# Kernel tuning notes

Measured on AMD Instinct MI355X. Metric: run time of the kernel, lower is better.

Reference implementation:

```python
import jax, jax.numpy as jnp
import numpy as np

NEG_SLOPE = 0.2


def setup_inputs() -> dict:
    key = jax.random.key(0)
    ks = jax.random.split(key, 9)
    N, E, D, H, C, G = 50000, 800000, 128, 4, 32, 64
    x = jax.random.normal(ks[0], (N, D), dtype=jnp.float32)
    edge_index = jax.random.randint(ks[1], (2, E), 0, N, dtype=jnp.int64)
    batch_ids = jnp.sort(jax.random.randint(ks[2], (N,), 0, G, dtype=jnp.int64))
    Wl = jax.random.normal(ks[3], (D, H * C), dtype=jnp.float32) / np.sqrt(D)
    Wr = jax.random.normal(ks[4], (D, H * C), dtype=jnp.float32) / np.sqrt(D)
    att = jax.random.normal(ks[5], (H, C), dtype=jnp.float32) / np.sqrt(C)
    bias_conv = jax.random.normal(ks[6], (H * C,), dtype=jnp.float32) * 0.01
    W_mlp = jax.random.normal(ks[7], (H * C, H * C), dtype=jnp.float32) / np.sqrt(H * C)
    b_mlp = jax.random.normal(ks[8], (H * C,), dtype=jnp.float32) * 0.01
    return {"x": x, "edge_index": edge_index, "batch_ids": batch_ids,
            "num_graphs": G, "Wl": Wl, "Wr": Wr, "att": att,
            "bias_conv": bias_conv, "W_mlp": W_mlp, "b_mlp": b_mlp}


def gatv2_forward(x, edge_index, batch_ids, num_graphs, Wl, Wr, att, bias_conv, W_mlp, b_mlp):
    N = x.shape[0]
    H, C = att.shape
    # add self loops (PyG default)
    loops = jnp.arange(N, dtype=edge_index.dtype)
    src = jnp.concatenate([edge_index[0], loops])
    dst = jnp.concatenate([edge_index[1], loops])
    xl = (x @ Wl).reshape(N, H, C)  # source transform
    xr = (x @ Wr).reshape(N, H, C)  # target transform
    # GATv2 attention logits per edge/head
    e = jax.nn.leaky_relu(xl[src] + xr[dst], NEG_SLOPE)  # [E,H,C]
    logits = jnp.einsum('ehc,hc->eh', e, att)            # [E,H]
    # segment softmax over incoming edges of each dst node
    m = jax.ops.segment_max(logits, dst, num_segments=N)
    ex = jnp.exp(logits - m[dst])
    denom = jax.ops.segment_sum(ex, dst, num_segments=N)
    alpha = ex / denom[dst]                              # [E,H]
    # weighted scatter-sum of source features
    out = jax.ops.segment_sum(alpha[:, :, None] * xl[src], dst, num_segments=N)
    out = out.reshape(N, H * C) + bias_conv
    out = jax.nn.relu(out)
    # global max pool per graph
    pooled = jax.ops.segment_max(out, batch_ids, num_segments=num_graphs)
    return jax.nn.relu(pooled @ W_mlp + b_mlp)


def reference(x, edge_index, batch_ids, num_graphs, Wl, Wr, att, bias_conv, W_mlp, b_mlp):
    return gatv2_forward(x, edge_index, batch_ids, num_graphs, Wl, Wr, att,
                         bias_conv, W_mlp, b_mlp)
```

## Files before the change

kernel.cpp:

```cpp
#include <hip/hip_runtime.h>
#include <hip/hip_bf16.h>

#define NN 50000
#define EE 800000
#define HC 128
#define GG 64

#define NBLK 256
#define CHUNK (EE / NBLK)
#define NBUCK ((NN + 63) >> 6)
#define NTOT (NBUCK * NBLK)
#define NSB ((NTOT + 1023) / 1024)
#define ECAP 2048

typedef __attribute__((ext_vector_type(8))) short bf16x8;
typedef __attribute__((ext_vector_type(4))) float f32x4;
typedef _Float16 hv2 __attribute__((ext_vector_type(2)));

__device__ __forceinline__ float dpp4_redrow(float t) {
  t += __int_as_float(__builtin_amdgcn_update_dpp(0, __float_as_int(t), 0x111, 0xf, 0xf, true));
  t += __int_as_float(__builtin_amdgcn_update_dpp(0, __float_as_int(t), 0x112, 0xf, 0xf, true));
  t += __int_as_float(__builtin_amdgcn_update_dpp(0, __float_as_int(t), 0x114, 0xf, 0xf, true));
  t += __int_as_float(__builtin_amdgcn_update_dpp(0, __float_as_int(t), 0x118, 0xf, 0xf, true));
  return t;
}
__device__ __forceinline__ float bcast15(float t) {
  return __int_as_float(__builtin_amdgcn_ds_swizzle(__float_as_int(t), 0x1F0));
}

__device__ __forceinline__ unsigned pkbf(float lo, float hi) {
  __hip_bfloat162 h = __float22bfloat162_rn(float2{lo, hi});
  return *reinterpret_cast<unsigned*>(&h);
}

__global__ __launch_bounds__(128) void prep_w(const float* __restrict__ Wl,
                                              const float* __restrict__ Wr,
                                              short* __restrict__ Wtb) {
  int c = blockIdx.x;
  int k = threadIdx.x;
  const float* W = (c < 128) ? Wl : Wr;
  float v = W[k * 128 + (c & 127)];
  Wtb[c * 128 + k] = (short)(pkbf(v, 0.f) & 0xFFFF);
}

__global__ __launch_bounds__(256) void gemm_xw(
    const float* __restrict__ x, const short* __restrict__ Wtb,
    _Float16* __restrict__ xlh, _Float16* __restrict__ xrh,
    const int* __restrict__ ei, int* __restrict__ H2T)
{
  __shared__ short xs[128 * 136];
  __shared__ int h[NBUCK];
  const int t = threadIdx.x;
  const int rowbase = blockIdx.x * 128;
#pragma unroll
  for (int i = 0; i < 16; ++i) {
    int fi = i * 256 + t;
    int row = fi >> 5, k4 = fi & 31;
    int ar = rowbase + row; if (ar >= NN) ar = NN - 1;
    float4 v = *(const float4*)(x + (size_t)ar * 128 + k4 * 4);
    uint2 p = { pkbf(v.x, v.y), pkbf(v.z, v.w) };
    *(uint2*)&xs[row * 136 + k4 * 4] = p;
  }
  __syncthreads();
  const int w = t >> 6, l = t & 63;
  const int lo16 = l & 15, hi = l >> 4;
  f32x4 accL[2][8], accR[2][8];
#pragma unroll
  for (int rf = 0; rf < 2; ++rf)
#pragma unroll
    for (int cf = 0; cf < 8; ++cf) {
      accL[rf][cf] = f32x4{0.f, 0.f, 0.f, 0.f};
      accR[rf][cf] = f32x4{0.f, 0.f, 0.f, 0.f};
    }

  const short* asrc0 = &xs[(w * 32 + lo16) * 136 + hi * 8];
  const short* asrc1 = asrc0 + 16 * 136;
#pragma unroll
  for (int ks = 0; ks < 4; ++ks) {
    bf16x8 a0 = *(const bf16x8*)(asrc0 + ks * 32);
    bf16x8 a1 = *(const bf16x8*)(asrc1 + ks * 32);
#pragma unroll
    for (int cf = 0; cf < 8; ++cf) {
      const short* bp = &Wtb[(cf * 16 + lo16) * 128 + ks * 32 + hi * 8];
      bf16x8 bL = *(const bf16x8*)bp;
      bf16x8 bR = *(const bf16x8*)(bp + 128 * 128);
      accL[0][cf] = __builtin_amdgcn_mfma_f32_16x16x32_bf16(a0, bL, accL[0][cf], 0, 0, 0);
      accL[1][cf] = __builtin_amdgcn_mfma_f32_16x16x32_bf16(a1, bL, accL[1][cf], 0, 0, 0);
      accR[0][cf] = __builtin_amdgcn_mfma_f32_16x16x32_bf16(a0, bR, accR[0][cf], 0, 0, 0);
      accR[1][cf] = __builtin_amdgcn_mfma_f32_16x16x32_bf16(a1, bR, accR[1][cf], 0, 0, 0);
    }
  }
#pragma unroll
  for (int rf = 0; rf < 2; ++rf)
#pragma unroll
    for (int cf = 0; cf < 8; ++cf)
#pragma unroll
      for (int r = 0; r < 4; ++r) {
        int row = rowbase + w * 32 + rf * 16 + hi * 4 + r;
        if (row < NN) {
          int col = cf * 16 + lo16;
          xlh[(size_t)row * 128 + col] = (_Float16)accL[rf][cf][r];
          xrh[(size_t)row * 128 + col] = (_Float16)accR[rf][cf][r];
        }
      }
  int blk = blockIdx.x;
  if (blk < NBLK) {
    for (int b = t; b < NBUCK; b += 256) h[b] = 0;
    __syncthreads();
    int e0 = blk * CHUNK;
    for (int i = t; i < CHUNK; i += 256) {
      int d = ei[EE + e0 + i];
      atomicAdd(&h[d >> 6], 1);
    }
    __syncthreads();
    for (int b = t; b < NBUCK; b += 256) H2T[b * NBLK + blk] = h[b];
  }
}

__global__ __launch_bounds__(256) void scanA(const int* __restrict__ H2T,
                                             int* __restrict__ PS, int* __restrict__ bsum) {
  __shared__ int tmp[256];
  int t = threadIdx.x;
  int base = blockIdx.x * 1024 + t * 4;
  int4 v = {0, 0, 0, 0};
  if (base < NTOT) v = *(const int4*)&H2T[base];
  int local = v.x + v.y + v.z + v.w;
  tmp[t] = local; __syncthreads();
  for (int off = 1; off < 256; off <<= 1) {
    int xv = (t >= off) ? tmp[t - off] : 0; __syncthreads();
    tmp[t] += xv; __syncthreads();
  }
  int excl = tmp[t] - local;
  if (base < NTOT) {
    int4 o;
    o.x = excl; excl += v.x;
    o.y = excl; excl += v.y;
    o.z = excl; excl += v.z;
    o.w = excl;
    *(int4*)&PS[base] = o;
  }
  if (t == 255) bsum[blockIdx.x] = tmp[255];
}

__global__ __launch_bounds__(256) void scatter_coarse(const int* __restrict__ ei,
                                                      const int* __restrict__ PS,
                                                      const int* __restrict__ bsum,
                                                      int* __restrict__ ec) {
  __shared__ int colbase[NBUCK];
  __shared__ int cur[NBUCK];
  __shared__ int sb[NSB];
  __shared__ int stmp[256];
  int t = threadIdx.x, blk = blockIdx.x;
  int v = (t < NSB) ? bsum[t] : 0;
  stmp[t] = v; __syncthreads();
  for (int off = 1; off < 256; off <<= 1) {
    int xv = (t >= off) ? stmp[t - off] : 0; __syncthreads();
    stmp[t] += xv; __syncthreads();
  }
  if (t < NSB) sb[t] = stmp[t] - v;
  __syncthreads();
  for (int b = t; b < NBUCK; b += 256) {
    int L = b * NBLK + blk;
    colbase[b] = PS[L] + sb[L >> 10];
    cur[b] = 0;
  }
  __syncthreads();
  int e0 = blk * CHUNK;
  for (int i = t; i < CHUNK; i += 256) {
    int d = ei[EE + e0 + i], s = ei[e0 + i];
    int b = d >> 6;
    int r = atomicAdd(&cur[b], 1);
    ec[colbase[b] + r] = s | ((d & 63) << 16);
  }
}

__global__ __launch_bounds__(256) void fine_sort(const int* __restrict__ PS,
                                                 const int* __restrict__ bsum,
                                                 const int* __restrict__ ec,
                                                 int* __restrict__ rs, int* __restrict__ csr) {
  __shared__ int lbuf[ECAP];
  __shared__ int outb[ECAP + 64];
  __shared__ int fh[64], sexcl[65], cur2[64];
  __shared__ int sb[NSB];
  __shared__ int stmp[256];
  int t = threadIdx.x, b = blockIdx.x;
  int v = (t < NSB) ? bsum[t] : 0;
  stmp[t] = v; __syncthreads();
  for (int off = 1; off < 256; off <<= 1) {
    int xv = (t >= off) ? stmp[t - off] : 0; __syncthreads();
    stmp[t] += xv; __syncthreads();
  }
  if (t < NSB) sb[t] = stmp[t] - v;
  __syncthreads();
  int L0 = b * NBLK;
  int start = PS[L0] + sb[L0 >> 10];
  int end = (b + 1 < NBUCK) ? PS[L0 + NBLK] + sb[(L0 + NBLK) >> 10] : EE;
  int node0 = b << 6;
  int nl = NN - node0; if (nl > 64) nl = 64;
  int cnt = end - start; if (cnt > ECAP) cnt = ECAP;
  if (t < 64) { fh[t] = 0; cur2[t] = 0; }
  __syncthreads();
  for (int i = t; i < cnt; i += 256) {
    int p = ec[start + i];
    lbuf[i] = p;
    atomicAdd(&fh[(p >> 16) & 63], 1);
  }
  __syncthreads();
  if (t < 64) {
    int val = fh[t] + (t < nl ? 1 : 0);
    int w = val;
    for (int off = 1; off < 64; off <<= 1) {
      int u = __shfl_up(w, off);
      if (t >= off) w += u;
    }
    sexcl[t] = w - val;
    if (t == 63) sexcl[64] = w;
  }
  __syncthreads();
  int base = start + node0;
  if (t <= nl) rs[node0 + t] = base + sexcl[t];
  if (t < nl) {
    int r = atomicAdd(&cur2[t], 1);
    outb[sexcl[t] + r] = node0 + t;
  }
  for (int i = t; i < cnt; i += 256) {
    int p = lbuf[i];
    int f = (p >> 16) & 63;
    int r = atomicAdd(&cur2[f], 1);
    outb[sexcl[f] + r] = p & 0xFFFF;
  }
  __syncthreads();
  int tot = cnt + nl;
  for (int i = t; i < tot; i += 256) csr[base + i] = outb[i];
}

template<int M>
__device__ __forceinline__ void procM(const unsigned* wv, hv2 att2, hv2 xr2,
                                      float& s, float& a0, float& a1) {
  float tb[M];
#pragma unroll
  for (int i = 0; i < M; ++i) {
    hv2 v = __builtin_bit_cast(hv2, wv[i]);
    hv2 y = v + xr2;
    hv2 lr = __builtin_elementwise_max(y, y * (_Float16)0.2f);
    float td = __builtin_amdgcn_fdot2(lr, att2, 0.f, false);
    tb[i] = bcast15(dpp4_redrow(td));
  }
  float p[M];
#pragma unroll
  for (int i = 0; i < M; ++i) p[i] = __builtin_amdgcn_exp2f(tb[i]);
#pragma unroll
  for (int i = 0; i < M; ++i) {
    hv2 v = __builtin_bit_cast(hv2, wv[i]);
    s += p[i];
    a0 = fmaf(p[i], (float)v.x, a0);
    a1 = fmaf(p[i], (float)v.y, a1);
  }
}

__global__ __launch_bounds__(256) void gat_agg(
    const unsigned* __restrict__ xlu, const unsigned* __restrict__ xru,
    const int* __restrict__ rs, const int* __restrict__ csr,
    const float* __restrict__ att, const float* __restrict__ bias,
    float* __restrict__ outn)
{
  int wid = threadIdx.x >> 6, lane = threadIdx.x & 63;
  int n = blockIdx.x * 4 + wid;
  if (n >= NN) return;
  hv2 xr2 = __builtin_bit_cast(hv2, xru[n * 64 + lane]);
  float2 at2 = ((const float2*)att)[lane];
  const float LOG2E = 1.4426950408889634f;
  hv2 att2;
  att2.x = (_Float16)(at2.x * LOG2E);
  att2.y = (_Float16)(at2.y * LOG2E);
  float s = 0.f, a0 = 0.f, a1 = 0.f;

  int jbeg = rs[n], jend = rs[n + 1];
  for (int j0 = jbeg; j0 < jend; j0 += 64) {
    int cnt = jend - j0; if (cnt > 64) cnt = 64;
    int sj = csr[j0 + (lane < cnt ? lane : cnt - 1)];
    int base = 0;
    if (cnt >= 8) {
      unsigned cur[8];
#pragma unroll
      for (int i = 0; i < 8; ++i)
        cur[i] = xlu[__builtin_amdgcn_readlane(sj, i) * 64 + lane];
      for (; base + 16 <= cnt; base += 8) {
        unsigned nxt[8];
#pragma unroll
        for (int i = 0; i < 8; ++i)
          nxt[i] = xlu[__builtin_amdgcn_readlane(sj, base + 8 + i) * 64 + lane];
        procM<8>(cur, att2, xr2, s, a0, a1);
#pragma unroll
        for (int i = 0; i < 8; ++i) cur[i] = nxt[i];
      }
      procM<8>(cur, att2, xr2, s, a0, a1);
      base += 8;
    }
    int rem = cnt - base;
    if (rem) {
      unsigned wv[8];
#pragma unroll
      for (int i = 0; i < 8; ++i)
        if (i < rem) wv[i] = xlu[__builtin_amdgcn_readlane(sj, base + i) * 64 + lane];
      switch (rem) {
        case 1: procM<1>(wv, att2, xr2, s, a0, a1); break;
        case 2: procM<2>(wv, att2, xr2, s, a0, a1); break;
        case 3: procM<3>(wv, att2, xr2, s, a0, a1); break;
        case 4: procM<4>(wv, att2, xr2, s, a0, a1); break;
        case 5: procM<5>(wv, att2, xr2, s, a0, a1); break;
        case 6: procM<6>(wv, att2, xr2, s, a0, a1); break;
        default: procM<7>(wv, att2, xr2, s, a0, a1); break;
      }
    }
  }
  float inv = 1.f / s;
  float2 bi = ((const float2*)bias)[lane];
  float2 o;
  o.x = fmaxf(fmaf(a0, inv, bi.x), 0.f);
  o.y = fmaxf(fmaf(a1, inv, bi.y), 0.f);
  ((float2*)outn)[n * 64 + lane] = o;
}

__global__ __launch_bounds__(1024) void pool_mlp(const float* __restrict__ outn,
                                                 const int* __restrict__ batch,
                                                 const float* __restrict__ W,
                                                 const float* __restrict__ bm,
                                                 float* __restrict__ out) {
  __shared__ float pm[8][128];
  __shared__ float p[128];
  __shared__ float acc8[8][128];
  int g = blockIdx.x, t = threadIdx.x;
  int c = t & 127, q = t >> 7;
  int a = 0, bnd = NN;
  while (a < bnd) { int m = (a + bnd) >> 1; if (batch[m] < g) a = m + 1; else bnd = m; }
  int lo = a;
  bnd = NN;
  while (a < bnd) { int m = (a + bnd) >> 1; if (batch[m] < g + 1) a = m + 1; else bnd = m; }
  int hi = a;
  float mx = 0.f;
#pragma unroll 4
  for (int n = lo + q; n < hi; n += 8) mx = fmaxf(mx, outn[(size_t)n * 128 + c]);
  pm[q][c] = mx;
  __syncthreads();
  if (q == 0) {
    float m0 = pm[0][c];
#pragma unroll
    for (int i = 1; i < 8; ++i) m0 = fmaxf(m0, pm[i][c]);
    p[c] = m0;
  }
  __syncthreads();
  float acc = 0.f;
#pragma unroll
  for (int kk = 0; kk < 16; ++kk) {
    int k = q * 16 + kk;
    acc = fmaf(p[k], W[k * 128 + c], acc);
  }
  acc8[q][c] = acc;
  __syncthreads();
  if (q == 0) {
    float sum = bm[c];
#pragma unroll
    for (int i = 0; i < 8; ++i) sum += acc8[i][c];
    out[g * 128 + c] = fmaxf(sum, 0.f);
  }
}

extern "C" void kernel_launch(void* const* d_in, const int* in_sizes, int n_in,
                              void* d_out, int out_size, void* d_ws, size_t ws_size,
                              hipStream_t stream) {
  const float* x    = (const float*)d_in[0];
  const int*   ei   = (const int*)d_in[1];
  const int*   batch= (const int*)d_in[2];
  const float* Wl   = (const float*)d_in[4];
  const float* Wr   = (const float*)d_in[5];
  const float* att  = (const float*)d_in[6];
  const float* bias = (const float*)d_in[7];
  const float* Wm   = (const float*)d_in[8];
  const float* bm   = (const float*)d_in[9];

  char* ws = (char*)d_ws;
  size_t off = 0;
  auto alloc = [&](size_t bytes) { void* p = ws + off; off += (bytes + 255) & ~size_t(255); return p; };
  unsigned* xlu  = (unsigned*)alloc((size_t)NN * 64 * 4);
  unsigned* xru  = (unsigned*)alloc((size_t)NN * 64 * 4);
  float* outn    = (float*)alloc((size_t)NN * HC * 4);
  int*   rs      = (int*)alloc((size_t)(NN + 1) * 4);
  int*   csr     = (int*)alloc((size_t)(EE + NN) * 4);
  int*   H2T     = (int*)alloc((size_t)NTOT * 4);
  int*   PS      = (int*)alloc((size_t)NTOT * 4);
  int*   ec      = (int*)alloc((size_t)EE * 4);
  int*   bsum    = (int*)alloc(NSB * 4);
  short* Wtb     = (short*)alloc((size_t)256 * 128 * 2);

  prep_w<<<256, 128, 0, stream>>>(Wl, Wr, Wtb);
  gemm_xw<<<(NN + 127) / 128, 256, 0, stream>>>(x, Wtb, (_Float16*)xlu, (_Float16*)xru, ei, H2T);
  scanA<<<NSB, 256, 0, stream>>>(H2T, PS, bsum);
  scatter_coarse<<<NBLK, 256, 0, stream>>>(ei, PS, bsum, ec);
  fine_sort<<<NBUCK, 256, 0, stream>>>(PS, bsum, ec, rs, csr);
  gat_agg<<<NN / 4, 256, 0, stream>>>(xlu, xru, rs, csr, att, bias, outn);
  pool_mlp<<<GG, 1024, 0, stream>>>(outn, batch, Wm, bm, (float*)d_out);
}
```

Measured before the change: 135.1 us.

## Store node outputs in fp16 and split pooling into parallel atomic max pass

The aggregation kernel now writes per-node outputs as packed fp16 rather than fp32, halving that intermediate's write and read traffic. The old one-block-per-graph pooling kernel is replaced by a kernel that spreads nodes across many small blocks and combines per-graph maxima with unsigned atomicMax. This relies on the values being non-negative after ReLU. A separate small kernel then does the MLP. The pooled buffer is zeroed inside prep_w. This trades an extra launch and fp16 rounding for more parallelism in pooling, which was limited to 64 blocks before.

```diff
diff --git a/kernel.cpp b/kernel.cpp
--- a/kernel.cpp
+++ b/kernel.cpp
@@ -32,15 +32,21 @@
   __hip_bfloat162 h = __float22bfloat162_rn(float2{lo, hi});
   return *reinterpret_cast<unsigned*>(&h);
 }
+__device__ __forceinline__ unsigned pkhf(float lo, float hi) {
+  hv2 h; h.x = (_Float16)lo; h.y = (_Float16)hi;
+  return __builtin_bit_cast(unsigned, h);
+}
 
 __global__ __launch_bounds__(128) void prep_w(const float* __restrict__ Wl,
                                               const float* __restrict__ Wr,
-                                              short* __restrict__ Wtb) {
+                                              short* __restrict__ Wtb,
+                                              unsigned* __restrict__ pooled) {
   int c = blockIdx.x;
   int k = threadIdx.x;
   const float* W = (c < 128) ? Wl : Wr;
   float v = W[k * 128 + (c & 127)];
   Wtb[c * 128 + k] = (short)(pkbf(v, 0.f) & 0xFFFF);
+  if (c < GG) pooled[c * 128 + k] = 0u;
 }
 
 __global__ __launch_bounds__(256) void gemm_xw(
@@ -262,7 +268,7 @@
     const unsigned* __restrict__ xlu, const unsigned* __restrict__ xru,
     const int* __restrict__ rs, const int* __restrict__ csr,
     const float* __restrict__ att, const float* __restrict__ bias,
-    float* __restrict__ outn)
+    unsigned* __restrict__ outh)
 {
   int wid = threadIdx.x >> 6, lane = threadIdx.x & 63;
   int n = blockIdx.x * 4 + wid;
@@ -316,54 +322,46 @@
   }
   float inv = 1.f / s;
   float2 bi = ((const float2*)bias)[lane];
-  float2 o;
-  o.x = fmaxf(fmaf(a0, inv, bi.x), 0.f);
-  o.y = fmaxf(fmaf(a1, inv, bi.y), 0.f);
-  ((float2*)outn)[n * 64 + lane] = o;
-}
-
-__global__ __launch_bounds__(1024) void pool_mlp(const float* __restrict__ outn,
-                                                 const int* __restrict__ batch,
-                                                 const float* __restrict__ W,
-                                                 const float* __restrict__ bm,
-                                                 float* __restrict__ out) {
-  __shared__ float pm[8][128];
+  float ox = fmaxf(fmaf(a0, inv, bi.x), 0.f);
+  float oy = fmaxf(fmaf(a1, inv, bi.y), 0.f);
+  outh[(size_t)n * 64 + lane] = pkhf(ox, oy);
+}
+
+__global__ __launch_bounds__(64) void pool_max(const unsigned* __restrict__ outh,
+                                               const int* __restrict__ batch,
+                                               unsigned* __restrict__ pooled) {
+  int c = threadIdx.x;
+  int n0 = blockIdx.x * 128;
+  int nend = n0 + 128; if (nend > NN) nend = NN;
+  int curg = batch[n0];
+  float m0 = 0.f, m1 = 0.f;
+  for (int n = n0; n < nend; ++n) {
+    int g = batch[n];
+    if (g != curg) {
+      atomicMax(&pooled[curg * 128 + 2 * c],     __float_as_uint(m0));
+      atomicMax(&pooled[curg * 128 + 2 * c + 1], __float_as_uint(m1));
+      m0 = m1 = 0.f; curg = g;
+    }
+    hv2 v = __builtin_bit_cast(hv2, outh[(size_t)n * 64 + c]);
+    m0 = fmaxf(m0, (float)v.x);
+    m1 = fmaxf(m1, (float)v.y);
+  }
+  atomicMax(&pooled[curg * 128 + 2 * c],     __float_as_uint(m0));
+  atomicMax(&pooled[curg * 128 + 2 * c + 1], __float_as_uint(m1));
+}
+
+__global__ __launch_bounds__(128) void mlp_out(const unsigned* __restrict__ pooled,
+                                               const float* __restrict__ W,
+                                               const float* __restrict__ b,
+                                               float* __restrict__ out) {
   __shared__ float p[128];
-  __shared__ float acc8[8][128];
-  int g = blockIdx.x, t = threadIdx.x;
-  int c = t & 127, q = t >> 7;
-  int a = 0, bnd = NN;
-  while (a < bnd) { int m = (a + bnd) >> 1; if (batch[m] < g) a = m + 1; else bnd = m; }
-  int lo = a;
-  bnd = NN;
-  while (a < bnd) { int m = (a + bnd) >> 1; if (batch[m] < g + 1) a = m + 1; else bnd = m; }
-  int hi = a;
-  float mx = 0.f;
-#pragma unroll 4
-  for (int n = lo + q; n < hi; n += 8) mx = fmaxf(mx, outn[(size_t)n * 128 + c]);
-  pm[q][c] = mx;
-  __syncthreads();
-  if (q == 0) {
-    float m0 = pm[0][c];
-#pragma unroll
-    for (int i = 1; i < 8; ++i) m0 = fmaxf(m0, pm[i][c]);
-    p[c] = m0;
-  }
-  __syncthreads();
-  float acc = 0.f;
-#pragma unroll
-  for (int kk = 0; kk < 16; ++kk) {
-    int k = q * 16 + kk;
-    acc = fmaf(p[k], W[k * 128 + c], acc);
-  }
-  acc8[q][c] = acc;
-  __syncthreads();
-  if (q == 0) {
-    float sum = bm[c];
-#pragma unroll
-    for (int i = 0; i < 8; ++i) sum += acc8[i][c];
-    out[g * 128 + c] = fmaxf(sum, 0.f);
-  }
+  int g = blockIdx.x, j = threadIdx.x;
+  p[j] = __uint_as_float(pooled[g * 128 + j]);
+  __syncthreads();
+  float acc = b[j];
+#pragma unroll 8
+  for (int k = 0; k < 128; ++k) acc = fmaf(p[k], W[k * 128 + j], acc);
+  out[g * 128 + j] = fmaxf(acc, 0.f);
 }
 
 extern "C" void kernel_launch(void* const* d_in, const int* in_sizes, int n_in,
@@ -384,7 +382,7 @@
   auto alloc = [&](size_t bytes) { void* p = ws + off; off += (bytes + 255) & ~size_t(255); return p; };
   unsigned* xlu  = (unsigned*)alloc((size_t)NN * 64 * 4);
   unsigned* xru  = (unsigned*)alloc((size_t)NN * 64 * 4);
-  float* outn    = (float*)alloc((size_t)NN * HC * 4);
+  unsigned* outh = (unsigned*)alloc((size_t)NN * 64 * 4);
   int*   rs      = (int*)alloc((size_t)(NN + 1) * 4);
   int*   csr     = (int*)alloc((size_t)(EE + NN) * 4);
   int*   H2T     = (int*)alloc((size_t)NTOT * 4);
@@ -392,12 +390,14 @@
   int*   ec      = (int*)alloc((size_t)EE * 4);
   int*   bsum    = (int*)alloc(NSB * 4);
   short* Wtb     = (short*)alloc((size_t)256 * 128 * 2);
-
-  prep_w<<<256, 128, 0, stream>>>(Wl, Wr, Wtb);
+  unsigned* pooled = (unsigned*)alloc((size_t)GG * 128 * 4);
+
+  prep_w<<<256, 128, 0, stream>>>(Wl, Wr, Wtb, pooled);
   gemm_xw<<<(NN + 127) / 128, 256, 0, stream>>>(x, Wtb, (_Float16*)xlu, (_Float16*)xru, ei, H2T);
   scanA<<<NSB, 256, 0, stream>>>(H2T, PS, bsum);
   scatter_coarse<<<NBLK, 256, 0, stream>>>(ei, PS, bsum, ec);
   fine_sort<<<NBUCK, 256, 0, stream>>>(PS, bsum, ec, rs, csr);
-  gat_agg<<<NN / 4, 256, 0, stream>>>(xlu, xru, rs, csr, att, bias, outn);
-  pool_mlp<<<GG, 1024, 0, stream>>>(outn, batch, Wm, bm, (float*)d_out);
-}
+  gat_agg<<<NN / 4, 256, 0, stream>>>(xlu, xru, rs, csr, att, bias, outh);
+  pool_max<<<(NN + 127) / 128, 64, 0, stream>>>(outh, batch, pooled);
+  mlp_out<<<GG, 128, 0, stream>>>(pooled, Wm, bm, (float*)d_out);
+}
```

Result: slower. 150.3 us (+11.3%).
